# Performance work log

Measured on AMD Instinct MI355X. Metric: run time of the kernel, lower is better.

The kernel has to match this reference:

```python
import math
import jax, jax.numpy as jnp
import numpy as np
from jax import lax

CELL_SIZE = 8
N_BINS = 9
SIGNED = False


def _conv3x3(x, k):
    # x: [N,1,H,W], k: [1,1,3,3]; padding=1 (SAME), stride 1
    return lax.conv_general_dilated(
        x, k, window_strides=(1, 1), padding=[(1, 1), (1, 1)],
        dimension_numbers=("NCHW", "OIHW", "NCHW"))


def setup_inputs() -> dict:
    key = jax.random.key(0)
    x = jax.random.uniform(key, (64, 1, 512, 512), dtype=jnp.float32)
    sobel_x = jnp.array([[-1., 0., 1.], [-2., 0., 2.], [-1., 0., 1.]],
                        dtype=jnp.float32).reshape(1, 1, 3, 3)
    sobel_y = jnp.array([[-1., -2., -1.], [0., 0., 0.], [1., 2., 1.]],
                        dtype=jnp.float32).reshape(1, 1, 3, 3)
    return {"x": x, "sobel_x": sobel_x, "sobel_y": sobel_y}


def reference(x, sobel_x, sobel_y):
    n, _, H, W = x.shape
    angle_range = 2 * math.pi if SIGNED else math.pi

    gx = _conv3x3(x, sobel_x)  # [N,1,H,W]
    gy = _conv3x3(x, sobel_y)
    mag = jnp.sqrt(gx * gx + gy * gy)          # [N,1,H,W]
    ang = jnp.arctan2(gx, gy)                  # note: atan2(gx, gy) as in source
    ang = ang + math.pi if SIGNED else jnp.abs(ang)
    bins = jnp.floor(ang / angle_range * (N_BINS - 1)).astype(jnp.int32)  # [N,1,H,W]

    # scatter_(dim=1): one-hot write of magnitudes into bin channel
    onehot = jax.nn.one_hot(bins[:, 0], N_BINS, axis=1, dtype=mag.dtype)  # [N,nb,H,W]
    out = onehot * mag                                                     # [N,nb,H,W]

    # AvgPool2d(cell,stride=cell) * cell**2 == sum over each cell
    cs = CELL_SIZE
    hog = out.reshape(n, N_BINS, H // cs, cs, W // cs, cs).sum(axis=(3, 5))
    return hog.reshape(-1)
```

## Files before the change

kernel.cpp:

```cpp
#include <hip/hip_runtime.h>
#include <math.h>

#define IMG_H 512
#define IMG_W 512
#define NB 9

__global__ __launch_bounds__(256, 4) void hog_kernel(const float* __restrict__ x,
                                                     float* __restrict__ out) {
#pragma clang fp contract(off)
    const int tid  = threadIdx.x;
    const int w    = tid >> 6;
    const int lane = tid & 63;
    const int cl   = lane & 15;
    const int qid  = lane >> 4;
    const int sr   = qid >> 1;
    const int sc   = qid & 1;

    const int cx = (w << 4) | cl;
    const int cy = blockIdx.x;
    const int n  = blockIdx.y;

    const float* img = x + (size_t)n * (IMG_H * IMG_W);
    const int x0 = (cx << 3) + (sc << 2);
    const int y0 = (cy << 3) + (sr << 2);

    float r[6][6];
#pragma unroll
    for (int i = 0; i < 6; ++i) {
        const int y = y0 - 1 + i;
        if (y < 0 || y >= IMG_H) {
#pragma unroll
            for (int j = 0; j < 6; ++j) r[i][j] = 0.0f;
        } else {
            const float* row = img + (size_t)y * IMG_W;
            const float4 p = *(const float4*)(row + x0);
            r[i][1] = p.x; r[i][2] = p.y; r[i][3] = p.z; r[i][4] = p.w;
            r[i][0] = (x0 == 0)           ? 0.0f : row[x0 - 1];
            r[i][5] = (x0 + 4 >= IMG_W)   ? 0.0f : row[x0 + 4];
        }
    }

    float accA[4], accB[4], acc8;
#pragma unroll
    for (int k = 0; k < 4; ++k) { accA[k] = 0.0f; accB[k] = 0.0f; }
    acc8 = 0.0f;

    const float PI_F = 3.14159274101257324f;
    const float T1F  = 0.41421356237309503f;
    const float T3F  = 2.41421356237309503f;
    const float KPI  = 2.54647909f;
    const float EPS  = 5e-5f;

#pragma unroll
    for (int ry = 0; ry < 4; ++ry) {
#pragma unroll
        for (int j = 0; j < 4; ++j) {
            const float A0 = r[ry][j],     A1 = r[ry][j + 1], A2 = r[ry][j + 2];
            const float B0 = r[ry + 1][j],                    B2 = r[ry + 1][j + 2];
            const float C0 = r[ry + 2][j], C1 = r[ry + 2][j + 1], C2 = r[ry + 2][j + 2];

            const float gx = ((-A0 + (A2 - 2.0f * B0)) + (2.0f * B2 - C0)) + C2;
            const float gy = (((-A0 - 2.0f * A1) + (-A2)) + (C0 + 2.0f * C1)) + C2;

            const float u = fabsf(gx);
            const float W = fabsf(gy);
            const float q = u * u + W * W;
            const float mag = sqrtf(q);

            const float b1 = W * T1F;
            const float b3 = W * T3F;
            const bool c1 = u > b1;
            const bool c2 = u > W;
            const bool c3 = u > b3;
            const bool s  = gy > 0.0f;

            const float KW = KPI * W;
            const float E  = EPS * q;
            const float md = fminf(fminf(fabsf(u - b1), fabsf(u - b3)),
                                   fminf(fabsf(u - W), u));
            const bool flag = md * KW < E;

            const float w0 = flag ? 0.0f : mag;
            const float wP = s ? w0 : 0.0f;
            const float wN = w0 - wP;
            const float p1 = c1 ? wP : 0.0f;
            const float p2 = c2 ? wP : 0.0f;
            const float p3 = c3 ? wP : 0.0f;
            const float n1 = c1 ? wN : 0.0f;
            const float n2 = c2 ? wN : 0.0f;
            const float n3 = c3 ? wN : 0.0f;
            accA[0] += wP - p1; accA[1] += p1 - p2;
            accA[2] += p2 - p3; accA[3] += p3;
            accB[0] += wN - n1; accB[1] += n1 - n2;
            accB[2] += n2 - n3; accB[3] += n3;

            if (flag) {
                const float angf = (float)atan2((double)u, (double)gy);
                const float tc = (float)((double)angf / (double)PI_F) * 8.0f;
                int bc = (int)tc;
                int bin = bc > 8 ? 8 : bc;
                float wA = mag;
                const float tn = roundf(tc);
                const int B = (int)tn;
                if (B >= 1 && B <= 8 && fabsf(tc - tn) < 4e-6f &&
                    mag <= 1.05f) {
                    const float hw = 0.5f * mag;
                    accA[0] += (B == 0) ? hw : 0.0f;
                    accA[1] += (B == 1) ? hw : 0.0f;
                    accA[2] += (B == 2) ? hw : 0.0f;
                    accA[3] += (B == 3) ? hw : 0.0f;
                    accB[3] += (B == 4) ? hw : 0.0f;
                    accB[2] += (B == 5) ? hw : 0.0f;
                    accB[1] += (B == 6) ? hw : 0.0f;
                    accB[0] += (B == 7) ? hw : 0.0f;
                    acc8    += (B == 8) ? hw : 0.0f;
                    bin = B - 1; wA = hw;
                }
                accA[0] += (bin == 0) ? wA : 0.0f;
                accA[1] += (bin == 1) ? wA : 0.0f;
                accA[2] += (bin == 2) ? wA : 0.0f;
                accA[3] += (bin == 3) ? wA : 0.0f;
                accB[3] += (bin == 4) ? wA : 0.0f;
                accB[2] += (bin == 5) ? wA : 0.0f;
                accB[1] += (bin == 6) ? wA : 0.0f;
                accB[0] += (bin == 7) ? wA : 0.0f;
                acc8    += (bin == 8) ? wA : 0.0f;
            }
        }
    }

    const float vals[NB] = {accA[0], accA[1], accA[2], accA[3],
                            accB[3], accB[2], accB[1], accB[0], acc8};
    float* o = out + (size_t)n * (NB * 64 * 64) + (size_t)cy * 64 + cx;
#pragma unroll
    for (int k = 0; k < NB; ++k) {
        float v = vals[k];
        v += __shfl_xor(v, 16, 64);
        v += __shfl_xor(v, 32, 64);
        if ((k & 3) == qid) o[(size_t)k * 4096] = v;
    }
}

extern "C" void kernel_launch(void* const* d_in, const int* in_sizes, int n_in,
                              void* d_out, int out_size, void* d_ws, size_t ws_size,
                              hipStream_t stream) {
    const float* x = (const float*)d_in[0];
    float* out = (float*)d_out;
    hog_kernel<<<dim3(64, 64, 1), dim3(256, 1, 1), 0, stream>>>(x, out);
}
```

Before: 119.1 us.

## Stage image rows in LDS and defer rare exact-atan2 fallback to a mask loop

Each block now loads its 10-row strip of the image into shared memory with coalesced float4 loads, and threads read their 6x6 neighbourhoods from LDS. This replaces the scattered per-thread global loads, including the unaligned single-float halo loads. The rare near-boundary pixels that need the exact double-precision atan2 are recorded in a bitmask and recomputed from LDS in a separate loop after the main pass. That keeps the expensive branch out of the unrolled loop and should lower register pressure. The cost is 20KB of LDS per block, which may limit occupancy, plus an extra __syncthreads.

```diff
diff --git a/kernel.cpp b/kernel.cpp
--- a/kernel.cpp
+++ b/kernel.cpp
@@ -21,23 +21,36 @@
     const int n  = blockIdx.y;
 
     const float* img = x + (size_t)n * (IMG_H * IMG_W);
-    const int x0 = (cx << 3) + (sc << 2);
-    const int y0 = (cy << 3) + (sr << 2);
+    const int x0    = (cx << 3) + (sc << 2);
+    const int ybase = (cy << 3) - 1;
 
-    float r[6][6];
+    __shared__ float lds[10][IMG_W];
+
+#pragma unroll
+    for (int i = 0; i < 5; ++i) {
+        const int idx = tid + (i << 8);
+        const int r   = idx >> 7;
+        const int c4  = idx & 127;
+        const int y   = ybase + r;
+        const bool valid = (y >= 0) && (y < IMG_H);
+        const float* gp = img + (size_t)(valid ? y : 0) * IMG_W + (c4 << 2);
+        float4 v = *(const float4*)gp;
+        if (!valid) v = make_float4(0.0f, 0.0f, 0.0f, 0.0f);
+        *(float4*)&lds[r][c4 << 2] = v;
+    }
+    __syncthreads();
+
+    float rw[6][6];
 #pragma unroll
     for (int i = 0; i < 6; ++i) {
-        const int y = y0 - 1 + i;
-        if (y < 0 || y >= IMG_H) {
-#pragma unroll
-            for (int j = 0; j < 6; ++j) r[i][j] = 0.0f;
-        } else {
-            const float* row = img + (size_t)y * IMG_W;
-            const float4 p = *(const float4*)(row + x0);
-            r[i][1] = p.x; r[i][2] = p.y; r[i][3] = p.z; r[i][4] = p.w;
-            r[i][0] = (x0 == 0)           ? 0.0f : row[x0 - 1];
-            r[i][5] = (x0 + 4 >= IMG_W)   ? 0.0f : row[x0 + 4];
-        }
+        const int lr = (sr << 2) + i;
+        const float4 m4 = *(const float4*)&lds[lr][x0];
+        rw[i][1] = m4.x; rw[i][2] = m4.y; rw[i][3] = m4.z; rw[i][4] = m4.w;
+        const float lv = lds[lr][(x0 == 0) ? 0 : x0 - 1];
+        rw[i][0] = (x0 == 0) ? 0.0f : lv;
+        const int xr = x0 + 4;
+        const float rv = lds[lr][(xr > IMG_W - 1) ? IMG_W - 1 : xr];
+        rw[i][5] = (xr > IMG_W - 1) ? 0.0f : rv;
     }
 
     float accA[4], accB[4], acc8;
@@ -51,13 +64,15 @@
     const float KPI  = 2.54647909f;
     const float EPS  = 5e-5f;
 
+    unsigned msk = 0u;
+
 #pragma unroll
     for (int ry = 0; ry < 4; ++ry) {
 #pragma unroll
         for (int j = 0; j < 4; ++j) {
-            const float A0 = r[ry][j],     A1 = r[ry][j + 1], A2 = r[ry][j + 2];
-            const float B0 = r[ry + 1][j],                    B2 = r[ry + 1][j + 2];
-            const float C0 = r[ry + 2][j], C1 = r[ry + 2][j + 1], C2 = r[ry + 2][j + 2];
+            const float A0 = rw[ry][j],     A1 = rw[ry][j + 1], A2 = rw[ry][j + 2];
+            const float B0 = rw[ry + 1][j],                     B2 = rw[ry + 1][j + 2];
+            const float C0 = rw[ry + 2][j], C1 = rw[ry + 2][j + 1], C2 = rw[ry + 2][j + 2];
 
             const float gx = ((-A0 + (A2 - 2.0f * B0)) + (2.0f * B2 - C0)) + C2;
             const float gy = (((-A0 - 2.0f * A1) + (-A2)) + (C0 + 2.0f * C1)) + C2;
@@ -79,6 +94,7 @@
             const float md = fminf(fminf(fabsf(u - b1), fabsf(u - b3)),
                                    fminf(fabsf(u - W), u));
             const bool flag = md * KW < E;
+            msk |= flag ? (1u << (ry * 4 + j)) : 0u;
 
             const float w0 = flag ? 0.0f : mag;
             const float wP = s ? w0 : 0.0f;
@@ -93,40 +109,65 @@
             accA[2] += p2 - p3; accA[3] += p3;
             accB[0] += wN - n1; accB[1] += n1 - n2;
             accB[2] += n2 - n3; accB[3] += n3;
+        }
+    }
 
-            if (flag) {
-                const float angf = (float)atan2((double)u, (double)gy);
-                const float tc = (float)((double)angf / (double)PI_F) * 8.0f;
-                int bc = (int)tc;
-                int bin = bc > 8 ? 8 : bc;
-                float wA = mag;
-                const float tn = roundf(tc);
-                const int B = (int)tn;
-                if (B >= 1 && B <= 8 && fabsf(tc - tn) < 4e-6f &&
-                    mag <= 1.05f) {
-                    const float hw = 0.5f * mag;
-                    accA[0] += (B == 0) ? hw : 0.0f;
-                    accA[1] += (B == 1) ? hw : 0.0f;
-                    accA[2] += (B == 2) ? hw : 0.0f;
-                    accA[3] += (B == 3) ? hw : 0.0f;
-                    accB[3] += (B == 4) ? hw : 0.0f;
-                    accB[2] += (B == 5) ? hw : 0.0f;
-                    accB[1] += (B == 6) ? hw : 0.0f;
-                    accB[0] += (B == 7) ? hw : 0.0f;
-                    acc8    += (B == 8) ? hw : 0.0f;
-                    bin = B - 1; wA = hw;
-                }
-                accA[0] += (bin == 0) ? wA : 0.0f;
-                accA[1] += (bin == 1) ? wA : 0.0f;
-                accA[2] += (bin == 2) ? wA : 0.0f;
-                accA[3] += (bin == 3) ? wA : 0.0f;
-                accB[3] += (bin == 4) ? wA : 0.0f;
-                accB[2] += (bin == 5) ? wA : 0.0f;
-                accB[1] += (bin == 6) ? wA : 0.0f;
-                accB[0] += (bin == 7) ? wA : 0.0f;
-                acc8    += (bin == 8) ? wA : 0.0f;
-            }
+    while (msk) {
+        const int p  = __builtin_ctz(msk); msk &= msk - 1;
+        const int py = p >> 2;
+        const int jx = p & 3;
+        const int lr = (sr << 2) + py;
+        const int cc = x0 + jx;
+        const int cL = (cc == 0) ? 0 : cc - 1;
+        const int cR = (cc == IMG_W - 1) ? IMG_W - 1 : cc + 1;
+        const bool eL = (cc == 0);
+        const bool eR = (cc == IMG_W - 1);
+
+        float A0 = lds[lr][cL];     A0 = eL ? 0.0f : A0;
+        const float A1 = lds[lr][cc];
+        float A2 = lds[lr][cR];     A2 = eR ? 0.0f : A2;
+        float B0 = lds[lr + 1][cL]; B0 = eL ? 0.0f : B0;
+        float B2 = lds[lr + 1][cR]; B2 = eR ? 0.0f : B2;
+        float C0 = lds[lr + 2][cL]; C0 = eL ? 0.0f : C0;
+        const float C1 = lds[lr + 2][cc];
+        float C2 = lds[lr + 2][cR]; C2 = eR ? 0.0f : C2;
+
+        const float gx = ((-A0 + (A2 - 2.0f * B0)) + (2.0f * B2 - C0)) + C2;
+        const float gy = (((-A0 - 2.0f * A1) + (-A2)) + (C0 + 2.0f * C1)) + C2;
+        const float u = fabsf(gx);
+        const float W = fabsf(gy);
+        const float q = u * u + W * W;
+        const float mag = sqrtf(q);
+
+        const float angf = (float)atan2((double)u, (double)gy);
+        const float tc = (float)((double)angf / (double)PI_F) * 8.0f;
+        int bc = (int)tc;
+        int bin = bc > 8 ? 8 : bc;
+        float wA = mag;
+        const float tn = roundf(tc);
+        const int B = (int)tn;
+        if (B >= 1 && B <= 8 && fabsf(tc - tn) < 4e-6f && mag <= 1.05f) {
+            const float hw = 0.5f * mag;
+            accA[0] += (B == 0) ? hw : 0.0f;
+            accA[1] += (B == 1) ? hw : 0.0f;
+            accA[2] += (B == 2) ? hw : 0.0f;
+            accA[3] += (B == 3) ? hw : 0.0f;
+            accB[3] += (B == 4) ? hw : 0.0f;
+            accB[2] += (B == 5) ? hw : 0.0f;
+            accB[1] += (B == 6) ? hw : 0.0f;
+            accB[0] += (B == 7) ? hw : 0.0f;
+            acc8    += (B == 8) ? hw : 0.0f;
+            bin = B - 1; wA = hw;
         }
+        accA[0] += (bin == 0) ? wA : 0.0f;
+        accA[1] += (bin == 1) ? wA : 0.0f;
+        accA[2] += (bin == 2) ? wA : 0.0f;
+        accA[3] += (bin == 3) ? wA : 0.0f;
+        accB[3] += (bin == 4) ? wA : 0.0f;
+        accB[2] += (bin == 5) ? wA : 0.0f;
+        accB[1] += (bin == 6) ? wA : 0.0f;
+        accB[0] += (bin == 7) ? wA : 0.0f;
+        acc8    += (bin == 8) ? wA : 0.0f;
     }
 
     const float vals[NB] = {accA[0], accA[1], accA[2], accA[3],
```

Measured after the change: 119.8 us. Within noise of the previous version (+0.6%).
